# Kernel tuning notes

Measured on AMD Instinct MI355X. Metric: run time of the kernel, lower is better.

Reference implementation:

```python
import jax, jax.numpy as jnp
import numpy as np

N_QUBITS = 12
N_LAYERS = 1
DIM = 1 << N_QUBITS
SUB_DIM = 1 << (N_QUBITS // 2)
# use_wscale=True, lrmul=1, gain=sqrt(2): init_std=1, w_mul = gain*5**-0.5
W_MUL = (2.0 ** 0.5) * (5.0 ** -0.5)


def _cnot_perm(n_qubits, n_layers):
    """Composite permutation of all CNOT gates (each CNOT permutes basis states).

    Applying gates g1..gk in sequence to a state v gives v_out[j] = v[p1(p2(...pk(j)))]
    (each CNOT perm is an involution). qubit 0 = most significant bit.
    """
    dim = 1 << n_qubits
    gates = []
    for _ in range(n_layers):
        for q in range(n_qubits - 1):
            gates.append((q, q + 1))
        gates.append((n_qubits - 1, 0))
    perm = np.arange(dim)
    for (c, t) in reversed(gates):
        bc = n_qubits - 1 - c
        bt = n_qubits - 1 - t
        perm = perm ^ (((perm >> bc) & 1) << bt)
    return perm

CNOT_PERM = _cnot_perm(N_QUBITS, N_LAYERS)


def _xyz_layer_unitary(w):
    """Kron of per-qubit Rz(w_z) @ Ry(w_y) @ Rx(w_x); w shape (3n,) float."""
    n = N_QUBITS
    tx, ty, tz = w[:n], w[n:2 * n], w[2 * n:3 * n]
    cx, sx = jnp.cos(tx / 2), jnp.sin(tx / 2)
    zero = jnp.zeros_like(cx)
    Rx = jnp.stack([jnp.stack([cx + 0j, -1j * sx], -1),
                    jnp.stack([-1j * sx, cx + 0j], -1)], -2)        # (n,2,2)
    cy, sy = jnp.cos(ty / 2), jnp.sin(ty / 2)
    Ry = jnp.stack([jnp.stack([cy + 0j, -sy + 0j], -1),
                    jnp.stack([sy + 0j, cy + 0j], -1)], -2)
    ez = jnp.exp(-1j * tz / 2)
    Rz = jnp.stack([jnp.stack([ez, zero + 0j], -1),
                    jnp.stack([zero + 0j, jnp.conj(ez)], -1)], -2)
    G = jnp.einsum('qab,qbc,qcd->qad', Rz, Ry, Rx)                  # (n,2,2)
    U = G[0]
    for q in range(1, n):
        U = jnp.kron(U, G[q])
    return U.astype(jnp.complex64)                                   # (DIM,DIM)


def _circuit_unitary(weight):
    w = (weight * W_MUL)[:3 * N_QUBITS]
    L = _xyz_layer_unitary(w)
    # U = L2 @ C @ L1 with L2 == L1 == L; C@L1 is a row gather by the CNOT perm
    return L @ L[CNOT_PERM, :]


def _evolve_and_ptrace(U, A, B, dA, dB):
    bsz = A.shape[0]
    # batched kron -> [B, DIM, DIM] complex density matrix
    rho = jnp.einsum('bij,bkl->bikjl', A, B).reshape(bsz, DIM, DIM).astype(jnp.complex64)
    out = U @ rho @ U.conj().T                                       # [B,DIM,DIM]
    out = out.reshape(bsz, dA, dB, dA, dB)
    return jnp.einsum('bikjk->bij', out)                             # Tr_B -> [B,dA,dA]


def setup_inputs() -> dict:
    key = jax.random.key(0)
    kA, kB, kW = jax.random.split(key, 3)
    inputA = jax.random.normal(kA, (2, SUB_DIM, SUB_DIM), dtype=jnp.float32)
    inputB = jax.random.normal(kB, (2, SUB_DIM, SUB_DIM), dtype=jnp.float32)
    weight = jax.random.uniform(kW, (6 * N_QUBITS,), dtype=jnp.float32) * (2 * np.pi)
    return {"inputA": inputA, "inputB": inputB, "weight": weight,
            "dimA": SUB_DIM, "dimB": SUB_DIM}


def reference(inputA, inputB, weight, dimA, dimB):
    assert dimA == dimB
    U = _circuit_unitary(weight)
    mutualBatA = _evolve_and_ptrace(U, inputA, inputB, dimA, dimB)
    mutualAatB = _evolve_and_ptrace(U, inputB, inputA, dimA, dimB)
    return (mutualBatA, mutualAatB)
```

## Files before the change

### kernel.cpp

```cpp
#include <hip/hip_runtime.h>
#include <hip/hip_bf16.h>


#define W_MUL 0.6324555320336759f

__device__ __forceinline__ float2 cmul(float2 a, float2 b) {
    return make_float2(a.x * b.x - a.y * b.y, a.x * b.y + a.y * b.x);
}
__device__ __forceinline__ float2 cadd(float2 a, float2 b) { return make_float2(a.x + b.x, a.y + b.y); }
__device__ __forceinline__ float2 csub(float2 a, float2 b) { return make_float2(a.x - b.x, a.y - b.y); }
__device__ __forceinline__ float2 conjc(float2 a) { return make_float2(a.x, -a.y); }
__device__ __forceinline__ float2 cfma(float2 a, float2 b, float2 c) {
    c.x = fmaf(a.x, b.x, fmaf(-a.y, b.y, c.x));
    c.y = fmaf(a.x, b.y, fmaf( a.y, b.x, c.y));
    return c;
}
__device__ __forceinline__ float2 cfmac(float2 a, float2 b, float2 c) {
    c.x = fmaf(a.x, b.x, fmaf( a.y, b.y, c.x));
    c.y = fmaf(a.x, b.y, fmaf(-a.y, b.x, c.y));
    return c;
}

__device__ __forceinline__ void make_G(const float* w, int q, float2 G[2][2]) {
    float tx = w[q]      * (W_MUL * 0.5f);
    float ty = w[12 + q] * (W_MUL * 0.5f);
    float tz = w[24 + q] * (W_MUL * 0.5f);
    float cx, sx, cy, sy, cz, sz;
    sincosf(tx, &sx, &cx);
    sincosf(ty, &sy, &cy);
    sincosf(tz, &sz, &cz);
    float2 M00 = make_float2( cy * cx,  sy * sx);
    float2 M01 = make_float2(-sy * cx, -cy * sx);
    float2 M10 = make_float2( sy * cx, -cy * sx);
    float2 M11 = make_float2( cy * cx, -sy * sx);
    float2 ez  = make_float2(cz, -sz);
    float2 ezc = make_float2(cz,  sz);
    G[0][0] = cmul(ez,  M00);
    G[0][1] = cmul(ez,  M01);
    G[1][0] = cmul(ezc, M10);
    G[1][1] = cmul(ezc, M11);
}

__device__ __forceinline__ void build_LH(const float2 G[6][2][2], float2* dst, int t, int nt) {
    for (int e = t; e < 4096; e += nt) {
        int i = e >> 6, j = e & 63;
        float2 p = G[0][(i >> 5) & 1][(j >> 5) & 1];
        p = cmul(p, G[1][(i >> 4) & 1][(j >> 4) & 1]);
        p = cmul(p, G[2][(i >> 3) & 1][(j >> 3) & 1]);
        p = cmul(p, G[3][(i >> 2) & 1][(j >> 2) & 1]);
        p = cmul(p, G[4][(i >> 1) & 1][(j >> 1) & 1]);
        p = cmul(p, G[5][(i     ) & 1][(j     ) & 1]);
        dst[j * 64 + i] = conjc(p);
    }
}

__device__ __forceinline__ void make_tables(const float2 G[6][2][2],
                                            float2 zt[6][2][2], float2 x6[2][2], float2 xz6[2][2]) {
    #pragma unroll
    for (int q = 0; q < 6; ++q)
        #pragma unroll
        for (int a = 0; a < 2; ++a)
            #pragma unroll
            for (int b = 0; b < 2; ++b) {
                float2 g0a = G[q][0][a], g0b = G[q][0][b];
                float2 g1a = G[q][1][a], g1b = G[q][1][b];
                zt[q][a][b] = csub(cmul(conjc(g0a), g0b), cmul(conjc(g1a), g1b));
                if (q == 0) {
                    x6[a][b]  = cadd(cmul(conjc(g0a), g1b), cmul(conjc(g1a), g0b));
                    xz6[a][b] = csub(cmul(conjc(g1a), g0b), cmul(conjc(g0a), g1b));
                }
            }
}

__device__ __forceinline__ void trace_acc(const float* Xr, const float2 zt[6][2][2],
                                          const float2 x6[2][2], const float2 xz6[2][2],
                                          int t, int nt, float acc[7]) {
    for (int e = t; e < 4096; e += nt) {
        int r = e >> 6, c = e & 63;
        float xv = Xr[e];
        float2 P = zt[1][(c >> 4) & 1][(r >> 4) & 1];
        P = cmul(P, zt[2][(c >> 3) & 1][(r >> 3) & 1]);
        P = cmul(P, zt[3][(c >> 2) & 1][(r >> 2) & 1]);
        P = cmul(P, zt[4][(c >> 1) & 1][(r >> 1) & 1]);
        P = cmul(P, zt[5][c & 1][r & 1]);
        float2 pz  = cmul(zt[0][c >> 5][r >> 5], P);
        float2 pxz = cmul(xz6[c >> 5][r >> 5], P);
        acc[0] = fmaf(pz.x,  xv, acc[0]); acc[1] = fmaf(pz.y,  xv, acc[1]);
        acc[2] = fmaf(pxz.x, xv, acc[2]); acc[3] = fmaf(pxz.y, xv, acc[3]);
        if ((c & 31) == (r & 31)) {
            float2 kx = x6[c >> 5][r >> 5];
            acc[4] = fmaf(kx.x, xv, acc[4]); acc[5] = fmaf(kx.y, xv, acc[5]);
            if (c == r) acc[6] += xv;
        }
    }
}

template <int NT>
__device__ __forceinline__ bool reduce7(float acc[7], float (*red)[8], int t) {
    #pragma unroll
    for (int o = 32; o; o >>= 1)
        #pragma unroll
        for (int m = 0; m < 7; ++m) acc[m] += __shfl_down(acc[m], o);
    if ((t & 63) == 0)
        for (int m = 0; m < 7; ++m) red[t >> 6][m] = acc[m];
    __syncthreads();
    if (t == 0) {
        for (int m = 0; m < 7; ++m) {
            float s = 0.f;
            for (int wv = 0; wv < NT / 64; ++wv) s += red[wv][m];
            acc[m] = s;
        }
        return true;
    }
    return false;
}

__device__ __forceinline__ void pick_cc(int p, int q, float2 e0, float2 e1, float2 f0, float2 f1,
                                        float2& c0, float2& c1) {
    if (p & 1) { if (q & 1) { c0 = e1; c1 = e0; } else { c0 = f1; c1 = f0; } }
    else       { if (q & 1) { c0 = f0; c1 = f1; } else { c0 = e0; c1 = e1; } }
}

__global__ __launch_bounds__(512) void qk1(const float* __restrict__ A, const float* __restrict__ B,
                                           const float* __restrict__ w, float2* __restrict__ ws) {
    __shared__ float2 LAH[4096];
    __shared__ float  Xr[4096];
    __shared__ float2 TMP[512];
    __shared__ float2 G6[6][2][2];
    __shared__ float  red[8][8];

    const int bx = blockIdx.x;
    const int t  = threadIdx.x;

    if (bx < 32) {
        const int x   = bx >> 3;
        const int oct = bx & 7;
        const float* Xg = (x < 2) ? (A + x * 4096) : (B + (x - 2) * 4096);
        if (t < 6) make_G(w, t, G6[t]);
        __syncthreads();
        build_LH(G6, LAH, t, 512);
        for (int e = t; e < 4096; e += 512) Xr[e] = Xg[e];
        __syncthreads();

        const int il = t >> 6;
        const int j  = t & 63;
        const int i  = (oct << 3) + il;

        float ax = 0.f, ay = 0.f;
        #pragma unroll 16
        for (int k = 0; k < 64; ++k) {
            float2 la = LAH[(k << 6) + i];
            float  xv = Xr[(k << 6) + j];
            ax = fmaf(la.x, xv, ax);
            ay = fmaf(-la.y, xv, ay);
        }
        TMP[(il << 6) + j] = make_float2(ax, ay);
        __syncthreads();

        float2 c = make_float2(0.f, 0.f);
        #pragma unroll 16
        for (int k = 0; k < 64; ++k)
            c = cfma(TMP[(il << 6) + k], LAH[(k << 6) + j], c);
        ws[(x << 12) + (i << 6) + j] = c;
    } else {
        const int x = bx - 32;
        const float* Xg = (x < 2) ? (A + x * 4096) : (B + (x - 2) * 4096);
        if (t < 6) make_G(w, 6 + t, G6[t]);
        for (int e = t; e < 4096; e += 512) Xr[e] = Xg[e];
        __syncthreads();
        float2 zt[6][2][2], x6[2][2], xz6[2][2];
        make_tables(G6, zt, x6, xz6);
        float acc[7] = {0, 0, 0, 0, 0, 0, 0};
        trace_acc(Xr, zt, x6, xz6, t, 512, acc);
        if (reduce7<512>(acc, red, t)) {
            float2* S = ws + 16384 + (x << 2);
            S[0] = make_float2(0.5f * (acc[6] + acc[0]),  0.5f * acc[1]);
            S[1] = make_float2(0.5f * (acc[6] - acc[0]), -0.5f * acc[1]);
            S[2] = make_float2(0.5f * (acc[4] + acc[2]),  0.5f * (acc[5] + acc[3]));
            S[3] = make_float2(0.5f * (acc[4] - acc[2]),  0.5f * (acc[5] - acc[3]));
        }
    }
}

template <int OM>
__global__ __launch_bounds__(512) void qk2(const float* __restrict__ w, const float2* __restrict__ ws,
                                           void* __restrict__ outv) {
    __shared__ float2 LAH[4096];
    __shared__ float2 A1s[4096];
    __shared__ float2 Ts[4096];
    __shared__ float2 Us[512];
    __shared__ float2 G6[6][2][2];

    const int bx = blockIdx.x;
    const int ev = bx >> 3, oct = bx & 7;
    const int order = ev >> 1, b = ev & 1;
    const int x1 = order ? 2 + b : b;
    const int x2 = order ? b : 2 + b;
    const int t = threadIdx.x;

    if (t < 6) make_G(w, t, G6[t]);
    __syncthreads();
    build_LH(G6, LAH, t, 512);
    for (int e = t; e < 4096; e += 512) A1s[e] = ws[(x1 << 12) + e];
    __syncthreads();

    const float2 e0 = ws[16384 + (x2 << 2) + 0];
    const float2 e1 = ws[16384 + (x2 << 2) + 1];
    const float2 f0 = ws[16384 + (x2 << 2) + 2];
    const float2 f1 = ws[16384 + (x2 << 2) + 3];

    for (int idx = t; idx < 4096; idx += 512) {
        int p = idx >> 6, q = idx & 63;
        int u = p ^ (p >> 1), v = q ^ (q >> 1);
        float2 c0, c1;
        pick_cc(p, q, e0, e1, f0, f1, c0, c1);
        float2 a  = A1s[(u << 6) + v];
        float2 a2 = A1s[((u ^ 48) << 6) + (v ^ 48)];
        Ts[idx] = cadd(cmul(a, c0), cmul(a2, c1));
    }
    __syncthreads();

    const int il = t >> 6;
    const int j  = t & 63;
    const int i  = (oct << 3) + il;

    float2 u = make_float2(0.f, 0.f);
    #pragma unroll 16
    for (int k = 0; k < 64; ++k)
        u = cfmac(LAH[(k << 6) + i], Ts[(k << 6) + j], u);
    Us[(il << 6) + j] = u;
    __syncthreads();

    float2 r = make_float2(0.f, 0.f);
    #pragma unroll 16
    for (int k = 0; k < 64; ++k)
        r = cfma(Us[(il << 6) + k], LAH[(k << 6) + j], r);

    if constexpr (OM == 0) {
        ((float*)outv)[(ev << 12) + (i << 6) + j] = r.x;
    } else if constexpr (OM == 1) {
        __hip_bfloat16* og = (__hip_bfloat16*)outv + (ev << 13) + (i << 7);
        og[2 * j]     = __float2bfloat16(r.x);
        og[2 * j + 1] = __float2bfloat16(r.y);
    } else {
        ((float2*)outv)[(ev << 12) + (i << 6) + j] = r;
    }
}

template <int OM>
__global__ __launch_bounds__(1024) void qfused(const float* __restrict__ A, const float* __restrict__ B,
                                               const float* __restrict__ w, void* __restrict__ outv) {
    __shared__ float2 LAH[4096];
    __shared__ float  Xr[4096];
    __shared__ float2 BA[4096];
    __shared__ float2 BB[4096];
    __shared__ float2 G6[6][2][2];
    __shared__ float  red[16][8];
    __shared__ float2 Sq[4];

    const int bx = blockIdx.x;
    const int ev = bx >> 2, rq = bx & 3;
    const int order = ev >> 1, b = ev & 1;
    const int t = threadIdx.x;
    const float* X1g = (order ? B : A) + b * 4096;
    const float* X2g = (order ? A : B) + b * 4096;

    if (t < 6) make_G(w, t, G6[t]);
    __syncthreads();
    build_LH(G6, LAH, t, 1024);
    for (int e = t; e < 4096; e += 1024) Xr[e] = X1g[e];
    __syncthreads();

    const int tr = t >> 5, tc = t & 31;
    const int i0 = tr, i1 = tr + 32;
    {
        float2 a00 = {0,0}, a01 = {0,0}, a10 = {0,0}, a11 = {0,0};
        #pragma unroll 16
        for (int k = 0; k < 64; ++k) {
            float2 la0 = LAH[(k << 6) + i0], la1 = LAH[(k << 6) + i1];
            float x0 = Xr[(k << 6) + tc], x1 = Xr[(k << 6) + tc + 32];
            a00.x = fmaf(la0.x, x0, a00.x); a00.y = fmaf(-la0.y, x0, a00.y);
            a01.x = fmaf(la0.x, x1, a01.x); a01.y = fmaf(-la0.y, x1, a01.y);
            a10.x = fmaf(la1.x, x0, a10.x); a10.y = fmaf(-la1.y, x0, a10.y);
            a11.x = fmaf(la1.x, x1, a11.x); a11.y = fmaf(-la1.y, x1, a11.y);
        }
        BA[(i0 << 6) + tc] = a00; BA[(i0 << 6) + tc + 32] = a01;
        BA[(i1 << 6) + tc] = a10; BA[(i1 << 6) + tc + 32] = a11;
    }
    __syncthreads();
    {
        float2 a00 = {0,0}, a01 = {0,0}, a10 = {0,0}, a11 = {0,0};
        #pragma unroll 16
        for (int k = 0; k < 64; ++k) {
            float2 t0 = BA[(i0 << 6) + k], t1 = BA[(i1 << 6) + k];
            float2 l0 = LAH[(k << 6) + tc], l1 = LAH[(k << 6) + tc + 32];
            a00 = cfma(t0, l0, a00); a01 = cfma(t0, l1, a01);
            a10 = cfma(t1, l0, a10); a11 = cfma(t1, l1, a11);
        }
        BB[(i0 << 6) + tc] = a00; BB[(i0 << 6) + tc + 32] = a01;
        BB[(i1 << 6) + tc] = a10; BB[(i1 << 6) + tc + 32] = a11;
    }
    __syncthreads();
    for (int e = t; e < 4096; e += 1024) Xr[e] = X2g[e];
    if (t < 6) make_G(w, 6 + t, G6[t]);
    __syncthreads();
    {
        float2 zt[6][2][2], x6[2][2], xz6[2][2];
        make_tables(G6, zt, x6, xz6);
        float acc[7] = {0, 0, 0, 0, 0, 0, 0};
        trace_acc(Xr, zt, x6, xz6, t, 1024, acc);
        if (reduce7<1024>(acc, red, t)) {
            Sq[0] = make_float2(0.5f * (acc[6] + acc[0]),  0.5f * acc[1]);
            Sq[1] = make_float2(0.5f * (acc[6] - acc[0]), -0.5f * acc[1]);
            Sq[2] = make_float2(0.5f * (acc[4] + acc[2]),  0.5f * (acc[5] + acc[3]));
            Sq[3] = make_float2(0.5f * (acc[4] - acc[2]),  0.5f * (acc[5] - acc[3]));
        }
    }
    __syncthreads();
    {
        const float2 e0 = Sq[0], e1 = Sq[1], f0 = Sq[2], f1 = Sq[3];
        for (int idx = t; idx < 4096; idx += 1024) {
            int p = idx >> 6, q = idx & 63;
            int u = p ^ (p >> 1), v = q ^ (q >> 1);
            float2 c0, c1;
            pick_cc(p, q, e0, e1, f0, f1, c0, c1);
            float2 a  = BB[(u << 6) + v];
            float2 a2 = BB[((u ^ 48) << 6) + (v ^ 48)];
            BA[idx] = cadd(cmul(a, c0), cmul(a2, c1));
        }
    }
    __syncthreads();
    const int il = t >> 6;
    const int i  = (rq << 4) + il;
    const int j  = t & 63;
    {
        float2 u = make_float2(0, 0);
        #pragma unroll 16
        for (int k = 0; k < 64; ++k)
            u = cfmac(LAH[(k << 6) + i], BA[(k << 6) + j], u);
        __syncthreads();
        BB[(il << 6) + j] = u;
    }
    __syncthreads();
    {
        float2 r = make_float2(0, 0);
        #pragma unroll 16
        for (int k = 0; k < 64; ++k)
            r = cfma(BB[(il << 6) + k], LAH[(k << 6) + j], r);
        if constexpr (OM == 0) {
            ((float*)outv)[(ev << 12) + (i << 6) + j] = r.x;
        } else if constexpr (OM == 1) {
            __hip_bfloat16* og = (__hip_bfloat16*)outv + (ev << 13) + (i << 7);
            og[2 * j]     = __float2bfloat16(r.x);
            og[2 * j + 1] = __float2bfloat16(r.y);
        } else {
            ((float2*)outv)[(ev << 12) + (i << 6) + j] = r;
        }
    }
}

extern "C" void kernel_launch(void* const* d_in, const int* in_sizes, int n_in,
                              void* d_out, int out_size, void* d_ws, size_t ws_size,
                              hipStream_t stream) {
    const float* A = (const float*)d_in[0];
    const float* B = (const float*)d_in[1];
    const float* w = (const float*)d_in[2];
    (void)in_sizes; (void)n_in;
    const bool two = (ws_size >= 16400u * sizeof(float2));
    if (two) {
        qk1<<<36, 512, 0, stream>>>(A, B, w, (float2*)d_ws);
        if (out_size == 16384)      qk2<0><<<32, 512, 0, stream>>>(w, (const float2*)d_ws, d_out);
        else if (out_size == 32768) qk2<1><<<32, 512, 0, stream>>>(w, (const float2*)d_ws, d_out);
        else                        qk2<2><<<32, 512, 0, stream>>>(w, (const float2*)d_ws, d_out);
    } else {
        if (out_size == 16384)      qfused<0><<<16, 1024, 0, stream>>>(A, B, w, d_out);
        else if (out_size == 32768) qfused<1><<<16, 1024, 0, stream>>>(A, B, w, d_out);
        else                        qfused<2><<<16, 1024, 0, stream>>>(A, B, w, d_out);
    }
}
```

Measured before the change: 81.30 us.

## Merge two-kernel pipeline into one cooperative kernel with grid sync

Replaces the qk1+qk2 launch pair with a single cooperative kernel that runs the first stage, does a grid-wide sync, then runs the second stage. It also reuses the LAH table already held in shared memory instead of rebuilding it in the second stage. This is meant to remove one kernel launch and the inter-kernel gap. In exchange it raises shared-memory use per block and adds the cost of a cooperative launch, and it falls back to the two kernels if the cooperative launch fails.

```diff
diff --git a/kernel.cpp b/kernel.cpp
--- a/kernel.cpp
+++ b/kernel.cpp
@@ -1,6 +1,9 @@
 #include <hip/hip_runtime.h>
 #include <hip/hip_bf16.h>
-
+#include <hip/hip_cooperative_groups.h>
+
+
+namespace cg = cooperative_groups;
 
 #define W_MUL 0.6324555320336759f
 
@@ -121,11 +124,29 @@
     else       { if (q & 1) { c0 = f0; c1 = f1; } else { c0 = e0; c1 = e1; } }
 }
 
-__global__ __launch_bounds__(512) void qk1(const float* __restrict__ A, const float* __restrict__ B,
-                                           const float* __restrict__ w, float2* __restrict__ ws) {
+template <int OM>
+__device__ __forceinline__ void write_one(void* outv, int ev, int i, int j, float2 r) {
+    if constexpr (OM == 0) {
+        ((float*)outv)[(ev << 12) + (i << 6) + j] = r.x;
+    } else if constexpr (OM == 1) {
+        __hip_bfloat16* og = (__hip_bfloat16*)outv + (ev << 13) + (i << 7);
+        og[2 * j]     = __float2bfloat16(r.x);
+        og[2 * j + 1] = __float2bfloat16(r.y);
+    } else {
+        ((float2*)outv)[(ev << 12) + (i << 6) + j] = r;
+    }
+}
+
+template <int OM>
+__global__ __launch_bounds__(512) void qcoop(const float* __restrict__ A, const float* __restrict__ B,
+                                             const float* __restrict__ w, void* __restrict__ outv,
+                                             float2* __restrict__ ws) {
     __shared__ float2 LAH[4096];
     __shared__ float  Xr[4096];
     __shared__ float2 TMP[512];
+    __shared__ float2 A1s[4096];
+    __shared__ float2 Ts[4096];
+    __shared__ float2 Us[512];
     __shared__ float2 G6[6][2][2];
     __shared__ float  red[8][8];
 
@@ -180,6 +201,110 @@
             S[3] = make_float2(0.5f * (acc[4] - acc[2]),  0.5f * (acc[5] - acc[3]));
         }
     }
+
+    __threadfence();
+    cg::this_grid().sync();
+
+    if (bx < 32) {
+        const int ev = bx >> 3, oct = bx & 7;
+        const int x2 = ev ^ 2;
+
+        for (int e = t; e < 4096; e += 512) A1s[e] = ws[(ev << 12) + e];
+        const float2 e0 = ws[16384 + (x2 << 2) + 0];
+        const float2 e1 = ws[16384 + (x2 << 2) + 1];
+        const float2 f0 = ws[16384 + (x2 << 2) + 2];
+        const float2 f1 = ws[16384 + (x2 << 2) + 3];
+        __syncthreads();
+
+        for (int idx = t; idx < 4096; idx += 512) {
+            int p = idx >> 6, q = idx & 63;
+            int u = p ^ (p >> 1), v = q ^ (q >> 1);
+            float2 c0, c1;
+            pick_cc(p, q, e0, e1, f0, f1, c0, c1);
+            float2 a  = A1s[(u << 6) + v];
+            float2 a2 = A1s[((u ^ 48) << 6) + (v ^ 48)];
+            Ts[idx] = cadd(cmul(a, c0), cmul(a2, c1));
+        }
+        __syncthreads();
+
+        const int il = t >> 6;
+        const int j  = t & 63;
+        const int i  = (oct << 3) + il;
+
+        float2 u = make_float2(0.f, 0.f);
+        #pragma unroll 16
+        for (int k = 0; k < 64; ++k)
+            u = cfmac(LAH[(k << 6) + i], Ts[(k << 6) + j], u);
+        Us[(il << 6) + j] = u;
+        __syncthreads();
+
+        float2 r = make_float2(0.f, 0.f);
+        #pragma unroll 16
+        for (int k = 0; k < 64; ++k)
+            r = cfma(Us[(il << 6) + k], LAH[(k << 6) + j], r);
+        write_one<OM>(outv, ev, i, j, r);
+    }
+}
+
+__global__ __launch_bounds__(512) void qk1(const float* __restrict__ A, const float* __restrict__ B,
+                                           const float* __restrict__ w, float2* __restrict__ ws) {
+    __shared__ float2 LAH[4096];
+    __shared__ float  Xr[4096];
+    __shared__ float2 TMP[512];
+    __shared__ float2 G6[6][2][2];
+    __shared__ float  red[8][8];
+
+    const int bx = blockIdx.x;
+    const int t  = threadIdx.x;
+
+    if (bx < 32) {
+        const int x   = bx >> 3;
+        const int oct = bx & 7;
+        const float* Xg = (x < 2) ? (A + x * 4096) : (B + (x - 2) * 4096);
+        if (t < 6) make_G(w, t, G6[t]);
+        __syncthreads();
+        build_LH(G6, LAH, t, 512);
+        for (int e = t; e < 4096; e += 512) Xr[e] = Xg[e];
+        __syncthreads();
+
+        const int il = t >> 6;
+        const int j  = t & 63;
+        const int i  = (oct << 3) + il;
+
+        float ax = 0.f, ay = 0.f;
+        #pragma unroll 16
+        for (int k = 0; k < 64; ++k) {
+            float2 la = LAH[(k << 6) + i];
+            float  xv = Xr[(k << 6) + j];
+            ax = fmaf(la.x, xv, ax);
+            ay = fmaf(-la.y, xv, ay);
+        }
+        TMP[(il << 6) + j] = make_float2(ax, ay);
+        __syncthreads();
+
+        float2 c = make_float2(0.f, 0.f);
+        #pragma unroll 16
+        for (int k = 0; k < 64; ++k)
+            c = cfma(TMP[(il << 6) + k], LAH[(k << 6) + j], c);
+        ws[(x << 12) + (i << 6) + j] = c;
+    } else {
+        const int x = bx - 32;
+        const float* Xg = (x < 2) ? (A + x * 4096) : (B + (x - 2) * 4096);
+        if (t < 6) make_G(w, 6 + t, G6[t]);
+        for (int e = t; e < 4096; e += 512) Xr[e] = Xg[e];
+        __syncthreads();
+        float2 zt[6][2][2], x6[2][2], xz6[2][2];
+        make_tables(G6, zt, x6, xz6);
+        float acc[7] = {0, 0, 0, 0, 0, 0, 0};
+        trace_acc(Xr, zt, x6, xz6, t, 512, acc);
+        if (reduce7<512>(acc, red, t)) {
+            float2* S = ws + 16384 + (x << 2);
+            S[0] = make_float2(0.5f * (acc[6] + acc[0]),  0.5f * acc[1]);
+            S[1] = make_float2(0.5f * (acc[6] - acc[0]), -0.5f * acc[1]);
+            S[2] = make_float2(0.5f * (acc[4] + acc[2]),  0.5f * (acc[5] + acc[3]));
+            S[3] = make_float2(0.5f * (acc[4] - acc[2]),  0.5f * (acc[5] - acc[3]));
+        }
+    }
 }
 
 template <int OM>
@@ -235,16 +360,7 @@
     #pragma unroll 16
     for (int k = 0; k < 64; ++k)
         r = cfma(Us[(il << 6) + k], LAH[(k << 6) + j], r);
-
-    if constexpr (OM == 0) {
-        ((float*)outv)[(ev << 12) + (i << 6) + j] = r.x;
-    } else if constexpr (OM == 1) {
-        __hip_bfloat16* og = (__hip_bfloat16*)outv + (ev << 13) + (i << 7);
-        og[2 * j]     = __float2bfloat16(r.x);
-        og[2 * j + 1] = __float2bfloat16(r.y);
-    } else {
-        ((float2*)outv)[(ev << 12) + (i << 6) + j] = r;
-    }
+    write_one<OM>(outv, ev, i, j, r);
 }
 
 template <int OM>
@@ -347,15 +463,26 @@
         #pragma unroll 16
         for (int k = 0; k < 64; ++k)
             r = cfma(BB[(il << 6) + k], LAH[(k << 6) + j], r);
-        if constexpr (OM == 0) {
-            ((float*)outv)[(ev << 12) + (i << 6) + j] = r.x;
-        } else if constexpr (OM == 1) {
-            __hip_bfloat16* og = (__hip_bfloat16*)outv + (ev << 13) + (i << 7);
-            og[2 * j]     = __float2bfloat16(r.x);
-            og[2 * j + 1] = __float2bfloat16(r.y);
-        } else {
-            ((float2*)outv)[(ev << 12) + (i << 6) + j] = r;
-        }
+        write_one<OM>(outv, ev, i, j, r);
+    }
+}
+
+template <int OM>
+static void launch_all(const float* A, const float* B, const float* w,
+                       void* d_out, void* d_ws, size_t ws_size, hipStream_t stream) {
+    const bool two = (ws_size >= 16400u * sizeof(float2));
+    if (two) {
+        const float* Aa = A; const float* Bb = B; const float* ww = w;
+        void* op = d_out; float2* wp = (float2*)d_ws;
+        void* args[] = { (void*)&Aa, (void*)&Bb, (void*)&ww, (void*)&op, (void*)&wp };
+        hipError_t err = hipLaunchCooperativeKernel(
+            reinterpret_cast<void*>(&qcoop<OM>), dim3(36), dim3(512), args, 0, stream);
+        if (err == hipSuccess) return;
+        (void)hipGetLastError();
+        qk1<<<36, 512, 0, stream>>>(A, B, w, (float2*)d_ws);
+        qk2<OM><<<32, 512, 0, stream>>>(w, (const float2*)d_ws, d_out);
+    } else {
+        qfused<OM><<<16, 1024, 0, stream>>>(A, B, w, d_out);
     }
 }
 
@@ -366,15 +493,7 @@
     const float* B = (const float*)d_in[1];
     const float* w = (const float*)d_in[2];
     (void)in_sizes; (void)n_in;
-    const bool two = (ws_size >= 16400u * sizeof(float2));
-    if (two) {
-        qk1<<<36, 512, 0, stream>>>(A, B, w, (float2*)d_ws);
-        if (out_size == 16384)      qk2<0><<<32, 512, 0, stream>>>(w, (const float2*)d_ws, d_out);
-        else if (out_size == 32768) qk2<1><<<32, 512, 0, stream>>>(w, (const float2*)d_ws, d_out);
-        else                        qk2<2><<<32, 512, 0, stream>>>(w, (const float2*)d_ws, d_out);
-    } else {
-        if (out_size == 16384)      qfused<0><<<16, 1024, 0, stream>>>(A, B, w, d_out);
-        else if (out_size == 32768) qfused<1><<<16, 1024, 0, stream>>>(A, B, w, d_out);
-        else                        qfused<2><<<16, 1024, 0, stream>>>(A, B, w, d_out);
-    }
-}
+    if (out_size == 16384)      launch_all<0>(A, B, w, d_out, d_ws, ws_size, stream);
+    else if (out_size == 32768) launch_all<1>(A, B, w, d_out, d_ws, ws_size, stream);
+    else                        launch_all<2>(A, B, w, d_out, d_ws, ws_size, stream);
+}
```

Measured after the change: 107.7 us. 1.33x slower.
